# Performance work log

Measured on AMD Instinct MI355X. Metric: run time of the kernel, lower is better.

The kernel has to match this reference:

```python
import jax, jax.numpy as jnp
import numpy as np

N, H, T, HID = 2, 8, 1024, 64
EMBED_DIM = H * HID  # 512, out_proj dim
EPS = 1e-6


def setup_inputs() -> dict:
    key = jax.random.key(0)
    kq, kk, kv, kw, kb = jax.random.split(key, 5)
    q = jax.random.normal(kq, (N, H, T, HID), jnp.float32)
    k = jax.random.normal(kk, (N, H, T, HID), jnp.float32)
    v = jax.random.normal(kv, (N, H, T, HID), jnp.float32)
    W_out = jax.random.normal(kw, (EMBED_DIM, EMBED_DIM), jnp.float32) / np.float32(np.sqrt(EMBED_DIM))
    b_out = jax.random.normal(kb, (EMBED_DIM,), jnp.float32) * 0.02
    return {"q": q, "k": k, "v": v, "W_out": W_out, "b_out": b_out}


def reference(q, k, v, W_out, b_out):
    # cosFormer attention, causal=True, act_fun='relu', has_outproj=True
    n, h, t, hid = q.shape
    nh = n * h
    m = t  # max(src_len, tgt_len)

    # q/k: permute(2,0,1,3).view(T,N,H*HID) -> relu -> view(-1,N*H,HID).transpose(0,1)
    # is equivalent to a direct reshape (N,H,T,HID)->(N*H,T,HID) since relu is elementwise.
    qr = jax.nn.relu(q).reshape(nh, t, hid)
    kr = jax.nn.relu(k).reshape(nh, t, hid)
    # v: original does v.view(-1, N*H, HID).transpose(0,1) WITHOUT permuting first
    # (reinterprets the (N,H,T,HID) buffer as (T, N*H, HID)); reproduce faithfully.
    vr = jnp.swapaxes(v.reshape(t, nh, hid), 0, 1)  # (NH, T, HID)

    # cos/sin position reweighting: weight_index = pi/2 * arange(1..m), used as /m
    idx = (np.float32(np.pi / 2) * jnp.arange(1, t + 1, dtype=q.dtype)) / m  # (T,)
    s = jnp.sin(idx)[None, :, None]
    c = jnp.cos(idx)[None, :, None]
    q_ = jnp.concatenate([qr * s, qr * c], axis=-1)  # (NH, T, 2*HID)
    k_ = jnp.concatenate([kr * s, kr * c], axis=-1)  # (NH, T, 2*HID)

    # causal path: cumulative outer products k_ (x) v, then contract with q_
    kv = jnp.einsum('nld,nlm->nldm', k_, vr)          # (NH, T, 2*HID, HID)
    kv_cum = jnp.cumsum(kv, axis=1)
    qkv = jnp.einsum('nld,nldm->nlm', q_, kv_cum)     # (NH, T, HID)
    k_cum = jnp.cumsum(k_, axis=1)
    denom = jnp.maximum(jnp.einsum('nld,nld->nl', q_, k_cum), EPS)
    attn = qkv / denom[..., None]                     # (NH, T, HID)

    # (NH,T,HID) -> (T,N,H*HID), out_proj, back to (N,H,T,HID)
    attn = jnp.swapaxes(attn, 0, 1).reshape(t, n, h * hid)
    attn = attn @ W_out.T + b_out
    context = attn.reshape(t, n, h, hid).transpose(1, 2, 0, 3)  # (N,H,T,HID)
    probs = jnp.zeros((n, h, t, t), q.dtype)
    return context, probs
```

## Files before the change

### kernel.cpp

```cpp
#include <hip/hip_runtime.h>

#define TSEQ 1024
#define HIDV 64
#define NHEADS 16
#define LCH 64
#define NCH 16
#define EMBED 512
#define CTX_FLOATS (NHEADS * TSEQ * HIDV)
#define EPSV 1e-6f
#define PIH 1.5707963267948966f

typedef short bf16x8 __attribute__((ext_vector_type(8)));
typedef float f32x4 __attribute__((ext_vector_type(4)));

__device__ __forceinline__ float relu_f(float x) { return fmaxf(x, 0.0f); }
__device__ __forceinline__ ushort f2bf(float f) {
    uint u = __float_as_uint(f);
    u += 0x7FFF + ((u >> 16) & 1);
    return (ushort)(u >> 16);
}
__device__ __forceinline__ float bf2f(ushort h) { return __uint_as_float(((uint)h) << 16); }
__device__ __forceinline__ uint pk2(float a, float b) {
    return (uint)f2bf(a) | ((uint)f2bf(b) << 16);
}

__global__ __launch_bounds__(256) void kA_chunksum(
    const float* __restrict__ K, const float* __restrict__ V,
    const float* __restrict__ W,
    ushort* __restrict__ S16, float* __restrict__ ksumws,
    ushort* __restrict__ W16, float4* __restrict__ probs4)
{
    __shared__ ushort kwT[128 * 88];
    __shared__ ushort vT1[32 * 88];
    const int bid = blockIdx.x;
    const int tid = threadIdx.x;

    {
        float4 z = make_float4(0.f, 0.f, 0.f, 0.f);
        size_t base = (size_t)bid * 2560 + tid;
        #pragma unroll
        for (int s = 0; s < 10; ++s) probs4[base + s * 256] = z;
    }
    {
        int g = bid * 128 + (tid & 127);
        if (tid < 128) {
            float4 w4 = *(const float4*)(W + (size_t)g * 4);
            *(uint2*)(W16 + (size_t)g * 4) = make_uint2(pk2(w4.x, w4.y), pk2(w4.z, w4.w));
        }
    }

    const int pair = bid >> 1, mh = bid & 1, m0b = mh * 32;
    const int b = pair >> 4, c = pair & 15;
    const int l0 = c * LCH;

    #pragma unroll
    for (int s = 0; s < 4; ++s) {
        int e = tid + s * 256;
        int i = e >> 4, d = (e & 15) * 4;
        float4 k4 = *(const float4*)(K + (size_t)(b * TSEQ + l0 + i) * HIDV + d);
        float si, ci;
        __sincosf(PIH * (float)(l0 + i + 1) * (1.0f / 1024.0f), &si, &ci);
        float kv[4] = {relu_f(k4.x), relu_f(k4.y), relu_f(k4.z), relu_f(k4.w)};
        #pragma unroll
        for (int j = 0; j < 4; ++j) {
            kwT[(d + j) * 88 + i] = f2bf(si * kv[j]);
            kwT[(d + 64 + j) * 88 + i] = f2bf(ci * kv[j]);
        }
    }
    #pragma unroll
    for (int s = 0; s < 2; ++s) {
        int e = tid + s * 256;
        int i = e >> 3, mf = (e & 7) * 4;
        float4 v4 = *(const float4*)(V + ((size_t)(l0 + i) * NHEADS + b) * HIDV + m0b + mf);
        vT1[(mf + 0) * 88 + i] = f2bf(v4.x);
        vT1[(mf + 1) * 88 + i] = f2bf(v4.y);
        vT1[(mf + 2) * 88 + i] = f2bf(v4.z);
        vT1[(mf + 3) * 88 + i] = f2bf(v4.w);
    }
    __syncthreads();

    const int w = tid >> 6, lane = tid & 63;
    const int quad = lane >> 4, l15 = lane & 15;

    bf16x8 bfv[2][2];
    #pragma unroll
    for (int mt = 0; mt < 2; ++mt)
        #pragma unroll
        for (int kk = 0; kk < 2; ++kk)
            bfv[mt][kk] = *(const bf16x8*)(vT1 + (mt * 16 + l15) * 88 + kk * 32 + quad * 8);

    f32x4 acc[2][2];
    #pragma unroll
    for (int ii = 0; ii < 2; ++ii)
        #pragma unroll
        for (int mt = 0; mt < 2; ++mt) acc[ii][mt] = (f32x4){0.f, 0.f, 0.f, 0.f};
    #pragma unroll
    for (int ii = 0; ii < 2; ++ii) {
        int itv = w + ii * 4;
        #pragma unroll
        for (int kk = 0; kk < 2; ++kk) {
            bf16x8 af = *(const bf16x8*)(kwT + (itv * 16 + l15) * 88 + kk * 32 + quad * 8);
            #pragma unroll
            for (int mt = 0; mt < 2; ++mt)
                acc[ii][mt] = __builtin_amdgcn_mfma_f32_16x16x32_bf16(af, bfv[mt][kk], acc[ii][mt], 0, 0, 0);
        }
    }
    ushort* SpT = S16 + (size_t)pair * 8192;
    #pragma unroll
    for (int ii = 0; ii < 2; ++ii)
        #pragma unroll
        for (int mt = 0; mt < 2; ++mt) {
            int m = m0b + mt * 16 + l15;
            int ddb = (w + ii * 4) * 16 + quad * 4;
            uint2 pk = make_uint2(pk2(acc[ii][mt][0], acc[ii][mt][1]),
                                  pk2(acc[ii][mt][2], acc[ii][mt][3]));
            *(uint2*)(SpT + m * 128 + ddb) = pk;
        }
    if (mh == 0 && tid < 128) {
        float ssum = 0.f;
        #pragma unroll
        for (int ss = 0; ss < 8; ++ss) {
            uint4 u = *(const uint4*)(kwT + tid * 88 + ss * 8);
            ssum += bf2f((ushort)(u.x & 0xffff)) + bf2f((ushort)(u.x >> 16));
            ssum += bf2f((ushort)(u.y & 0xffff)) + bf2f((ushort)(u.y >> 16));
            ssum += bf2f((ushort)(u.z & 0xffff)) + bf2f((ushort)(u.z >> 16));
            ssum += bf2f((ushort)(u.w & 0xffff)) + bf2f((ushort)(u.w >> 16));
        }
        ksumws[(size_t)pair * 128 + tid] = ssum;
    }
}

#define SMEM_BYTES 58368
#define OFF_QW 0
#define OFF_KW 17408
#define OFF_PT 34816
#define OFF_VT 43520
#define OFF_AM 48128
#define OFF_PSUM 57344
#define OFF_DENA 57856
#define OFF_DENI 58112

__global__ __launch_bounds__(256) void kB_attn(
    const float* __restrict__ Q, const float* __restrict__ K,
    const float* __restrict__ V,
    const ushort* __restrict__ S16, const float* __restrict__ ksumws,
    ushort* __restrict__ attn216, float4* __restrict__ probs4)
{
    __shared__ __align__(16) char smem[SMEM_BYTES];
    ushort* qw = (ushort*)(smem + OFF_QW);
    ushort* kw = (ushort*)(smem + OFF_KW);
    ushort* Pt = (ushort*)(smem + OFF_PT);
    ushort* vT = (ushort*)(smem + OFF_VT);
    ushort* Am = (ushort*)(smem + OFF_AM);
    float* psum = (float*)(smem + OFF_PSUM);
    float* denA = (float*)(smem + OFF_DENA);
    float* denI = (float*)(smem + OFF_DENI);

    const int bid = blockIdx.x;
    const int tid = threadIdx.x;
    const int w = tid >> 6, lane = tid & 63;
    const int quad = lane >> 4, l15 = lane & 15;

    {
        float4 z = make_float4(0.f, 0.f, 0.f, 0.f);
        size_t base = 1310720 + (size_t)bid * 2560 + tid;
        #pragma unroll
        for (int s = 0; s < 10; ++s) probs4[base + s * 256] = z;
    }

    const int pair = bid >> 1, mh = bid & 1, m0b = mh * 32;
    const int b = pair >> 4, c = pair & 15;
    const int l0 = c * LCH;

    {
        const int ml = tid >> 3, dd0 = (tid & 7) * 16;
        const ushort* Sb = S16 + ((size_t)b * NCH) * 8192 + (m0b + ml) * 128 + dd0;
        float accp[16];
        #pragma unroll
        for (int u = 0; u < 16; ++u) accp[u] = 0.f;
        for (int cp = 0; cp < c; ++cp) {
            const ushort* Sp = Sb + (size_t)cp * 8192;
            uint4 u0 = *(const uint4*)(Sp);
            uint4 u1 = *(const uint4*)(Sp + 8);
            uint uu[8] = {u0.x, u0.y, u0.z, u0.w, u1.x, u1.y, u1.z, u1.w};
            #pragma unroll
            for (int p = 0; p < 8; ++p) {
                accp[p * 2 + 0] += bf2f((ushort)(uu[p] & 0xffff));
                accp[p * 2 + 1] += bf2f((ushort)(uu[p] >> 16));
            }
        }
        uint pkv[8];
        #pragma unroll
        for (int p = 0; p < 8; ++p) pkv[p] = pk2(accp[p * 2], accp[p * 2 + 1]);
        *(uint4*)(Pt + ml * 136 + dd0) = make_uint4(pkv[0], pkv[1], pkv[2], pkv[3]);
        *(uint4*)(Pt + ml * 136 + dd0 + 8) = make_uint4(pkv[4], pkv[5], pkv[6], pkv[7]);
    }
    if (tid < 128) {
        float s = 0.f;
        const float* Kb = ksumws + (size_t)b * NCH * 128 + tid;
        for (int cp = 0; cp < c; ++cp) s += Kb[cp * 128];
        psum[tid] = s;
    }

    #pragma unroll
    for (int s = 0; s < 4; ++s) {
        int e = tid + s * 256;
        int i = e >> 4, d = (e & 15) * 4;
        float si, ci;
        __sincosf(PIH * (float)(l0 + i + 1) * (1.0f / 1024.0f), &si, &ci);
        float4 q4 = *(const float4*)(Q + (size_t)(b * TSEQ + l0 + i) * HIDV + d);
        float qv[4] = {relu_f(q4.x), relu_f(q4.y), relu_f(q4.z), relu_f(q4.w)};
        *(uint2*)(qw + i * 136 + d) = make_uint2(pk2(si * qv[0], si * qv[1]), pk2(si * qv[2], si * qv[3]));
        *(uint2*)(qw + i * 136 + 64 + d) = make_uint2(pk2(ci * qv[0], ci * qv[1]), pk2(ci * qv[2], ci * qv[3]));
        float4 k4 = *(const float4*)(K + (size_t)(b * TSEQ + l0 + i) * HIDV + d);
        float kv[4] = {relu_f(k4.x), relu_f(k4.y), relu_f(k4.z), relu_f(k4.w)};
        *(uint2*)(kw + i * 136 + d) = make_uint2(pk2(si * kv[0], si * kv[1]), pk2(si * kv[2], si * kv[3]));
        *(uint2*)(kw + i * 136 + 64 + d) = make_uint2(pk2(ci * kv[0], ci * kv[1]), pk2(ci * kv[2], ci * kv[3]));
    }
    #pragma unroll
    for (int s = 0; s < 2; ++s) {
        int e = tid + s * 256;
        int j = e >> 3, mf = (e & 7) * 4;
        float4 v4 = *(const float4*)(V + ((size_t)(l0 + j) * NHEADS + b) * HIDV + m0b + mf);
        vT[(mf + 0) * 72 + j] = f2bf(v4.x);
        vT[(mf + 1) * 72 + j] = f2bf(v4.y);
        vT[(mf + 2) * 72 + j] = f2bf(v4.z);
        vT[(mf + 3) * 72 + j] = f2bf(v4.w);
    }
    __syncthreads();

    const int it = w;
    bf16x8 af[4];
    #pragma unroll
    for (int kk = 0; kk < 4; ++kk)
        af[kk] = *(const bf16x8*)(qw + (it * 16 + l15) * 136 + kk * 32 + quad * 8);

    f32x4 accA[4];
    #pragma unroll
    for (int jt = 0; jt < 4; ++jt) {
        accA[jt] = (f32x4){0.f, 0.f, 0.f, 0.f};
        #pragma unroll
        for (int kk = 0; kk < 4; ++kk) {
            bf16x8 bf = *(const bf16x8*)(kw + (jt * 16 + l15) * 136 + kk * 32 + quad * 8);
            accA[jt] = __builtin_amdgcn_mfma_f32_16x16x32_bf16(af[kk], bf, accA[jt], 0, 0, 0);
        }
    }
    {
        float rsum[4] = {0.f, 0.f, 0.f, 0.f};
        #pragma unroll
        for (int jt = 0; jt < 4; ++jt) {
            int j = jt * 16 + l15;
            #pragma unroll
            for (int r = 0; r < 4; ++r) {
                int i = it * 16 + quad * 4 + r;
                float val = (j <= i) ? accA[jt][r] : 0.f;
                Am[i * 72 + j] = f2bf(val);
                rsum[r] += val;
            }
        }
        #pragma unroll
        for (int off = 1; off < 16; off <<= 1) {
            rsum[0] += __shfl_xor(rsum[0], off);
            rsum[1] += __shfl_xor(rsum[1], off);
            rsum[2] += __shfl_xor(rsum[2], off);
            rsum[3] += __shfl_xor(rsum[3], off);
        }
        if (l15 == 0) {
            #pragma unroll
            for (int r = 0; r < 4; ++r) denA[it * 16 + quad * 4 + r] = rsum[r];
        }
    }
    if (tid < 64) {
        float s = 0.f;
        #pragma unroll
        for (int ss = 0; ss < 16; ++ss) {
            uint4 u = *(const uint4*)(qw + tid * 136 + ss * 8);
            s += bf2f((ushort)(u.x & 0xffff)) * psum[ss * 8 + 0] + bf2f((ushort)(u.x >> 16)) * psum[ss * 8 + 1];
            s += bf2f((ushort)(u.y & 0xffff)) * psum[ss * 8 + 2] + bf2f((ushort)(u.y >> 16)) * psum[ss * 8 + 3];
            s += bf2f((ushort)(u.z & 0xffff)) * psum[ss * 8 + 4] + bf2f((ushort)(u.z >> 16)) * psum[ss * 8 + 5];
            s += bf2f((ushort)(u.w & 0xffff)) * psum[ss * 8 + 6] + bf2f((ushort)(u.w >> 16)) * psum[ss * 8 + 7];
        }
        denI[tid] = s;
    }
    __syncthreads();

    f32x4 accO[2];
    #pragma unroll
    for (int mm = 0; mm < 2; ++mm) {
        accO[mm] = (f32x4){0.f, 0.f, 0.f, 0.f};
        #pragma unroll
        for (int kk = 0; kk < 4; ++kk) {
            bf16x8 bp = *(const bf16x8*)(Pt + (mm * 16 + l15) * 136 + kk * 32 + quad * 8);
            accO[mm] = __builtin_amdgcn_mfma_f32_16x16x32_bf16(af[kk], bp, accO[mm], 0, 0, 0);
        }
    }
    bf16x8 aA[2];
    #pragma unroll
    for (int kk = 0; kk < 2; ++kk)
        aA[kk] = *(const bf16x8*)(Am + (it * 16 + l15) * 72 + kk * 32 + quad * 8);
    #pragma unroll
    for (int mm = 0; mm < 2; ++mm)
        #pragma unroll
        for (int kk = 0; kk < 2; ++kk) {
            bf16x8 bv = *(const bf16x8*)(vT + (mm * 16 + l15) * 72 + kk * 32 + quad * 8);
            accO[mm] = __builtin_amdgcn_mfma_f32_16x16x32_bf16(aA[kk], bv, accO[mm], 0, 0, 0);
        }

    const int nb = b >> 3, hh = b & 7;
    #pragma unroll
    for (int r = 0; r < 4; ++r) {
        int i = it * 16 + quad * 4 + r;
        float inv = 1.0f / fmaxf(denA[i] + denI[i], EPSV);
        #pragma unroll
        for (int mm = 0; mm < 2; ++mm) {
            int m = m0b + mm * 16 + l15;
            attn216[(size_t)((l0 + i) * 2 + nb) * EMBED + hh * 64 + m] = f2bf(accO[mm][r] * inv);
        }
    }
}

__global__ __launch_bounds__(256) void kC_outproj(
    const ushort* __restrict__ A16, const ushort* __restrict__ W16,
    const float* __restrict__ bias, float* __restrict__ out,
    float4* __restrict__ probs4)
{
    __shared__ ushort Ab[32 * 72];
    __shared__ ushort Bb[64 * 72];
    const int bid = blockIdx.x;
    const int tid = threadIdx.x;
    {
        float4 z = make_float4(0.f, 0.f, 0.f, 0.f);
        size_t base = 2621440 + (size_t)bid * 3072 + tid;
        #pragma unroll
        for (int s = 0; s < 12; ++s) probs4[base + s * 256] = z;
    }
    const int rt = bid >> 3, et = bid & 7;
    const int r0 = rt * 32, e0 = et * 64;
    const int w = tid >> 6, lane = tid & 63;
    const int quad = lane >> 4, l15 = lane & 15;
    const int it4 = w >> 1, jt0 = (w & 1) * 2;
    f32x4 acc4[2];
    acc4[0] = (f32x4){0.f, 0.f, 0.f, 0.f};
    acc4[1] = (f32x4){0.f, 0.f, 0.f, 0.f};

    for (int f0 = 0; f0 < EMBED; f0 += 64) {
        __syncthreads();
        {
            int rr = tid >> 3, ff = (tid & 7) * 8;
            *(uint4*)(Ab + rr * 72 + ff) = *(const uint4*)(A16 + (size_t)(r0 + rr) * EMBED + f0 + ff);
        }
        #pragma unroll
        for (int s = 0; s < 2; ++s) {
            int e = tid + s * 256;
            int rr = e >> 3, ff = (e & 7) * 8;
            *(uint4*)(Bb + rr * 72 + ff) = *(const uint4*)(W16 + (size_t)(e0 + rr) * EMBED + f0 + ff);
        }
        __syncthreads();
        bf16x8 af2[2];
        #pragma unroll
        for (int kk = 0; kk < 2; ++kk)
            af2[kk] = *(const bf16x8*)(Ab + (it4 * 16 + l15) * 72 + kk * 32 + quad * 8);
        #pragma unroll
        for (int jj = 0; jj < 2; ++jj) {
            int jt = jt0 + jj;
            #pragma unroll
            for (int kk = 0; kk < 2; ++kk) {
                bf16x8 bf = *(const bf16x8*)(Bb + (jt * 16 + l15) * 72 + kk * 32 + quad * 8);
                acc4[jj] = __builtin_amdgcn_mfma_f32_16x16x32_bf16(af2[kk], bf, acc4[jj], 0, 0, 0);
            }
        }
    }
    #pragma unroll
    for (int jj = 0; jj < 2; ++jj) {
        int e = e0 + (jt0 + jj) * 16 + l15;
        float be = bias[e];
        int h = e >> 6, m = e & 63;
        #pragma unroll
        for (int r = 0; r < 4; ++r) {
            int rr = r0 + it4 * 16 + quad * 4 + r;
            int t = rr >> 1, n = rr & 1;
            out[((size_t)(n * 8 + h) * TSEQ + t) * HIDV + m] = acc4[jj][r] + be;
        }
    }
}

extern "C" void kernel_launch(void* const* d_in, const int* in_sizes, int n_in,
                              void* d_out, int out_size, void* d_ws, size_t ws_size,
                              hipStream_t stream) {
    const float* q = (const float*)d_in[0];
    const float* k = (const float*)d_in[1];
    const float* v = (const float*)d_in[2];
    const float* W = (const float*)d_in[3];
    const float* bias = (const float*)d_in[4];
    float* out = (float*)d_out;
    float* ws = (float*)d_ws;

    ushort* S16 = (ushort*)ws;
    float* ksum_ws = ws + 1048576;
    ushort* attn216 = (ushort*)(ws + 1081344);
    ushort* W16 = (ushort*)(ws + 1605632);
    float4* probs4 = (float4*)(out + CTX_FLOATS);

    kA_chunksum<<<dim3(512), dim3(256), 0, stream>>>(k, v, W, S16, ksum_ws, W16, probs4);
    kB_attn<<<dim3(512), dim3(256), 0, stream>>>(q, k, v, S16, ksum_ws, attn216, probs4);
    kC_outproj<<<dim3(512), dim3(256), 0, stream>>>(attn216, W16, bias, out, probs4);
}
```

Measured before the change: 115.0 us.

## Fuse three kernels into one cooperative kernel with grid syncs

Merges the chunk-sum, attention and out-projection kernels into a single cooperative launch, separated by grid.sync barriers. The K/Q/V tiles stay in LDS between the chunk-sum and attention phases instead of being reloaded. Attention output is staged through LDS so global stores are coalesced, and the zero-fill of probs and the final outputs use nontemporal stores. This removes two kernel launch gaps and the redundant K/V loads, but adds grid-wide barrier costs and requires all 512 blocks to be resident at once (launch_bounds 256,2).

Result: slower. 331.6 us (+188.3%).

```diff
diff --git a/kernel.cpp b/kernel.cpp
--- a/kernel.cpp
+++ b/kernel.cpp
@@ -1,4 +1,7 @@
 #include <hip/hip_runtime.h>
+#include <hip/hip_cooperative_groups.h>
+
+namespace cg = cooperative_groups;
 
 #define TSEQ 1024
 #define HIDV 64
@@ -24,22 +27,46 @@
     return (uint)f2bf(a) | ((uint)f2bf(b) << 16);
 }
 
-__global__ __launch_bounds__(256) void kA_chunksum(
-    const float* __restrict__ K, const float* __restrict__ V,
-    const float* __restrict__ W,
+#define LDS_BYTES 62976
+#define OFF_KW   0
+#define OFF_VT   17408
+#define OFF_R3   23040
+#define OFF_R4   45568
+#define OFF_PT   (OFF_R3 + 0)
+#define OFF_AM   (OFF_R3 + 8704)
+#define OFF_PSUM (OFF_R3 + 17920)
+#define OFF_DENA (OFF_R3 + 18432)
+#define OFF_DENI (OFF_R3 + 18688)
+
+__global__ __launch_bounds__(256, 2) void kFused(
+    const float* __restrict__ Q, const float* __restrict__ K,
+    const float* __restrict__ V, const float* __restrict__ W,
+    const float* __restrict__ bias,
     ushort* __restrict__ S16, float* __restrict__ ksumws,
-    ushort* __restrict__ W16, float4* __restrict__ probs4)
+    ushort* __restrict__ attn216, ushort* __restrict__ W16,
+    float* __restrict__ out, float4* __restrict__ probs4)
 {
-    __shared__ ushort kwT[128 * 88];
-    __shared__ ushort vT1[32 * 88];
+    __shared__ __align__(16) char smem[LDS_BYTES];
+    ushort* kw = (ushort*)(smem + OFF_KW);
+    ushort* vT = (ushort*)(smem + OFF_VT);
+    ushort* qw = (ushort*)(smem + OFF_R4);
+
     const int bid = blockIdx.x;
     const int tid = threadIdx.x;
-
-    {
-        float4 z = make_float4(0.f, 0.f, 0.f, 0.f);
+    const int w = tid >> 6, lane = tid & 63;
+    const int quad = lane >> 4, l15 = lane & 15;
+    const int pair = bid >> 1, mh = bid & 1, m0b = mh * 32;
+    const int b = pair >> 4, c = pair & 15;
+    const int l0 = c * LCH;
+
+    cg::grid_group grid = cg::this_grid();
+
+    {
+        f32x4 z = {0.f, 0.f, 0.f, 0.f};
         size_t base = (size_t)bid * 2560 + tid;
         #pragma unroll
-        for (int s = 0; s < 10; ++s) probs4[base + s * 256] = z;
+        for (int s = 0; s < 10; ++s)
+            __builtin_nontemporal_store(z, (f32x4*)&probs4[base + s * 256]);
     }
     {
         int g = bid * 128 + (tid & 127);
@@ -48,338 +75,289 @@
             *(uint2*)(W16 + (size_t)g * 4) = make_uint2(pk2(w4.x, w4.y), pk2(w4.z, w4.w));
         }
     }
-
-    const int pair = bid >> 1, mh = bid & 1, m0b = mh * 32;
-    const int b = pair >> 4, c = pair & 15;
-    const int l0 = c * LCH;
-
-    #pragma unroll
-    for (int s = 0; s < 4; ++s) {
-        int e = tid + s * 256;
-        int i = e >> 4, d = (e & 15) * 4;
-        float4 k4 = *(const float4*)(K + (size_t)(b * TSEQ + l0 + i) * HIDV + d);
-        float si, ci;
-        __sincosf(PIH * (float)(l0 + i + 1) * (1.0f / 1024.0f), &si, &ci);
-        float kv[4] = {relu_f(k4.x), relu_f(k4.y), relu_f(k4.z), relu_f(k4.w)};
-        #pragma unroll
-        for (int j = 0; j < 4; ++j) {
-            kwT[(d + j) * 88 + i] = f2bf(si * kv[j]);
-            kwT[(d + 64 + j) * 88 + i] = f2bf(ci * kv[j]);
-        }
-    }
-    #pragma unroll
-    for (int s = 0; s < 2; ++s) {
-        int e = tid + s * 256;
-        int i = e >> 3, mf = (e & 7) * 4;
-        float4 v4 = *(const float4*)(V + ((size_t)(l0 + i) * NHEADS + b) * HIDV + m0b + mf);
-        vT1[(mf + 0) * 88 + i] = f2bf(v4.x);
-        vT1[(mf + 1) * 88 + i] = f2bf(v4.y);
-        vT1[(mf + 2) * 88 + i] = f2bf(v4.z);
-        vT1[(mf + 3) * 88 + i] = f2bf(v4.w);
-    }
-    __syncthreads();
-
-    const int w = tid >> 6, lane = tid & 63;
-    const int quad = lane >> 4, l15 = lane & 15;
-
-    bf16x8 bfv[2][2];
-    #pragma unroll
-    for (int mt = 0; mt < 2; ++mt)
-        #pragma unroll
-        for (int kk = 0; kk < 2; ++kk)
-            bfv[mt][kk] = *(const bf16x8*)(vT1 + (mt * 16 + l15) * 88 + kk * 32 + quad * 8);
-
-    f32x4 acc[2][2];
-    #pragma unroll
-    for (int ii = 0; ii < 2; ++ii)
-        #pragma unroll
-        for (int mt = 0; mt < 2; ++mt) acc[ii][mt] = (f32x4){0.f, 0.f, 0.f, 0.f};
-    #pragma unroll
-    for (int ii = 0; ii < 2; ++ii) {
-        int itv = w + ii * 4;
-        #pragma unroll
-        for (int kk = 0; kk < 2; ++kk) {
-            bf16x8 af = *(const bf16x8*)(kwT + (itv * 16 + l15) * 88 + kk * 32 + quad * 8);
-            #pragma unroll
-            for (int mt = 0; mt < 2; ++mt)
-                acc[ii][mt] = __builtin_amdgcn_mfma_f32_16x16x32_bf16(af, bfv[mt][kk], acc[ii][mt], 0, 0, 0);
-        }
-    }
-    ushort* SpT = S16 + (size_t)pair * 8192;
-    #pragma unroll
-    for (int ii = 0; ii < 2; ++ii)
-        #pragma unroll
-        for (int mt = 0; mt < 2; ++mt) {
-            int m = m0b + mt * 16 + l15;
-            int ddb = (w + ii * 4) * 16 + quad * 4;
-            uint2 pk = make_uint2(pk2(acc[ii][mt][0], acc[ii][mt][1]),
-                                  pk2(acc[ii][mt][2], acc[ii][mt][3]));
-            *(uint2*)(SpT + m * 128 + ddb) = pk;
-        }
-    if (mh == 0 && tid < 128) {
-        float ssum = 0.f;
-        #pragma unroll
-        for (int ss = 0; ss < 8; ++ss) {
-            uint4 u = *(const uint4*)(kwT + tid * 88 + ss * 8);
-            ssum += bf2f((ushort)(u.x & 0xffff)) + bf2f((ushort)(u.x >> 16));
-            ssum += bf2f((ushort)(u.y & 0xffff)) + bf2f((ushort)(u.y >> 16));
-            ssum += bf2f((ushort)(u.z & 0xffff)) + bf2f((ushort)(u.z >> 16));
-            ssum += bf2f((ushort)(u.w & 0xffff)) + bf2f((ushort)(u.w >> 16));
-        }
-        ksumws[(size_t)pair * 128 + tid] = ssum;
-    }
-}
-
-#define SMEM_BYTES 58368
-#define OFF_QW 0
-#define OFF_KW 17408
-#define OFF_PT 34816
-#define OFF_VT 43520
-#define OFF_AM 48128
-#define OFF_PSUM 57344
-#define OFF_DENA 57856
-#define OFF_DENI 58112
-
-__global__ __launch_bounds__(256) void kB_attn(
-    const float* __restrict__ Q, const float* __restrict__ K,
-    const float* __restrict__ V,
-    const ushort* __restrict__ S16, const float* __restrict__ ksumws,
-    ushort* __restrict__ attn216, float4* __restrict__ probs4)
-{
-    __shared__ __align__(16) char smem[SMEM_BYTES];
-    ushort* qw = (ushort*)(smem + OFF_QW);
-    ushort* kw = (ushort*)(smem + OFF_KW);
-    ushort* Pt = (ushort*)(smem + OFF_PT);
-    ushort* vT = (ushort*)(smem + OFF_VT);
-    ushort* Am = (ushort*)(smem + OFF_AM);
-    float* psum = (float*)(smem + OFF_PSUM);
-    float* denA = (float*)(smem + OFF_DENA);
-    float* denI = (float*)(smem + OFF_DENI);
-
-    const int bid = blockIdx.x;
-    const int tid = threadIdx.x;
-    const int w = tid >> 6, lane = tid & 63;
-    const int quad = lane >> 4, l15 = lane & 15;
-
-    {
-        float4 z = make_float4(0.f, 0.f, 0.f, 0.f);
-        size_t base = 1310720 + (size_t)bid * 2560 + tid;
-        #pragma unroll
-        for (int s = 0; s < 10; ++s) probs4[base + s * 256] = z;
-    }
-
-    const int pair = bid >> 1, mh = bid & 1, m0b = mh * 32;
-    const int b = pair >> 4, c = pair & 15;
-    const int l0 = c * LCH;
-
-    {
-        const int ml = tid >> 3, dd0 = (tid & 7) * 16;
-        const ushort* Sb = S16 + ((size_t)b * NCH) * 8192 + (m0b + ml) * 128 + dd0;
-        float accp[16];
-        #pragma unroll
-        for (int u = 0; u < 16; ++u) accp[u] = 0.f;
-        for (int cp = 0; cp < c; ++cp) {
-            const ushort* Sp = Sb + (size_t)cp * 8192;
-            uint4 u0 = *(const uint4*)(Sp);
-            uint4 u1 = *(const uint4*)(Sp + 8);
-            uint uu[8] = {u0.x, u0.y, u0.z, u0.w, u1.x, u1.y, u1.z, u1.w};
-            #pragma unroll
-            for (int p = 0; p < 8; ++p) {
-                accp[p * 2 + 0] += bf2f((ushort)(uu[p] & 0xffff));
-                accp[p * 2 + 1] += bf2f((ushort)(uu[p] >> 16));
-            }
-        }
-        uint pkv[8];
-        #pragma unroll
-        for (int p = 0; p < 8; ++p) pkv[p] = pk2(accp[p * 2], accp[p * 2 + 1]);
-        *(uint4*)(Pt + ml * 136 + dd0) = make_uint4(pkv[0], pkv[1], pkv[2], pkv[3]);
-        *(uint4*)(Pt + ml * 136 + dd0 + 8) = make_uint4(pkv[4], pkv[5], pkv[6], pkv[7]);
-    }
-    if (tid < 128) {
-        float s = 0.f;
-        const float* Kb = ksumws + (size_t)b * NCH * 128 + tid;
-        for (int cp = 0; cp < c; ++cp) s += Kb[cp * 128];
-        psum[tid] = s;
-    }
-
-    #pragma unroll
-    for (int s = 0; s < 4; ++s) {
-        int e = tid + s * 256;
-        int i = e >> 4, d = (e & 15) * 4;
-        float si, ci;
-        __sincosf(PIH * (float)(l0 + i + 1) * (1.0f / 1024.0f), &si, &ci);
-        float4 q4 = *(const float4*)(Q + (size_t)(b * TSEQ + l0 + i) * HIDV + d);
-        float qv[4] = {relu_f(q4.x), relu_f(q4.y), relu_f(q4.z), relu_f(q4.w)};
-        *(uint2*)(qw + i * 136 + d) = make_uint2(pk2(si * qv[0], si * qv[1]), pk2(si * qv[2], si * qv[3]));
-        *(uint2*)(qw + i * 136 + 64 + d) = make_uint2(pk2(ci * qv[0], ci * qv[1]), pk2(ci * qv[2], ci * qv[3]));
-        float4 k4 = *(const float4*)(K + (size_t)(b * TSEQ + l0 + i) * HIDV + d);
-        float kv[4] = {relu_f(k4.x), relu_f(k4.y), relu_f(k4.z), relu_f(k4.w)};
-        *(uint2*)(kw + i * 136 + d) = make_uint2(pk2(si * kv[0], si * kv[1]), pk2(si * kv[2], si * kv[3]));
-        *(uint2*)(kw + i * 136 + 64 + d) = make_uint2(pk2(ci * kv[0], ci * kv[1]), pk2(ci * kv[2], ci * kv[3]));
-    }
-    #pragma unroll
-    for (int s = 0; s < 2; ++s) {
-        int e = tid + s * 256;
-        int j = e >> 3, mf = (e & 7) * 4;
-        float4 v4 = *(const float4*)(V + ((size_t)(l0 + j) * NHEADS + b) * HIDV + m0b + mf);
-        vT[(mf + 0) * 72 + j] = f2bf(v4.x);
-        vT[(mf + 1) * 72 + j] = f2bf(v4.y);
-        vT[(mf + 2) * 72 + j] = f2bf(v4.z);
-        vT[(mf + 3) * 72 + j] = f2bf(v4.w);
-    }
-    __syncthreads();
-
-    const int it = w;
-    bf16x8 af[4];
-    #pragma unroll
-    for (int kk = 0; kk < 4; ++kk)
-        af[kk] = *(const bf16x8*)(qw + (it * 16 + l15) * 136 + kk * 32 + quad * 8);
-
-    f32x4 accA[4];
-    #pragma unroll
-    for (int jt = 0; jt < 4; ++jt) {
-        accA[jt] = (f32x4){0.f, 0.f, 0.f, 0.f};
-        #pragma unroll
-        for (int kk = 0; kk < 4; ++kk) {
-            bf16x8 bf = *(const bf16x8*)(kw + (jt * 16 + l15) * 136 + kk * 32 + quad * 8);
-            accA[jt] = __builtin_amdgcn_mfma_f32_16x16x32_bf16(af[kk], bf, accA[jt], 0, 0, 0);
-        }
-    }
-    {
-        float rsum[4] = {0.f, 0.f, 0.f, 0.f};
-        #pragma unroll
-        for (int jt = 0; jt < 4; ++jt) {
-            int j = jt * 16 + l15;
-            #pragma unroll
-            for (int r = 0; r < 4; ++r) {
-                int i = it * 16 + quad * 4 + r;
-                float val = (j <= i) ? accA[jt][r] : 0.f;
-                Am[i * 72 + j] = f2bf(val);
-                rsum[r] += val;
-            }
-        }
-        #pragma unroll
-        for (int off = 1; off < 16; off <<= 1) {
-            rsum[0] += __shfl_xor(rsum[0], off);
-            rsum[1] += __shfl_xor(rsum[1], off);
-            rsum[2] += __shfl_xor(rsum[2], off);
-            rsum[3] += __shfl_xor(rsum[3], off);
-        }
-        if (l15 == 0) {
-            #pragma unroll
-            for (int r = 0; r < 4; ++r) denA[it * 16 + quad * 4 + r] = rsum[r];
-        }
-    }
-    if (tid < 64) {
-        float s = 0.f;
-        #pragma unroll
-        for (int ss = 0; ss < 16; ++ss) {
-            uint4 u = *(const uint4*)(qw + tid * 136 + ss * 8);
-            s += bf2f((ushort)(u.x & 0xffff)) * psum[ss * 8 + 0] + bf2f((ushort)(u.x >> 16)) * psum[ss * 8 + 1];
-            s += bf2f((ushort)(u.y & 0xffff)) * psum[ss * 8 + 2] + bf2f((ushort)(u.y >> 16)) * psum[ss * 8 + 3];
-            s += bf2f((ushort)(u.z & 0xffff)) * psum[ss * 8 + 4] + bf2f((ushort)(u.z >> 16)) * psum[ss * 8 + 5];
-            s += bf2f((ushort)(u.w & 0xffff)) * psum[ss * 8 + 6] + bf2f((ushort)(u.w >> 16)) * psum[ss * 8 + 7];
-        }
-        denI[tid] = s;
-    }
-    __syncthreads();
-
-    f32x4 accO[2];
-    #pragma unroll
-    for (int mm = 0; mm < 2; ++mm) {
-        accO[mm] = (f32x4){0.f, 0.f, 0.f, 0.f};
-        #pragma unroll
-        for (int kk = 0; kk < 4; ++kk) {
-            bf16x8 bp = *(const bf16x8*)(Pt + (mm * 16 + l15) * 136 + kk * 32 + quad * 8);
-            accO[mm] = __builtin_amdgcn_mfma_f32_16x16x32_bf16(af[kk], bp, accO[mm], 0, 0, 0);
-        }
-    }
-    bf16x8 aA[2];
-    #pragma unroll
-    for (int kk = 0; kk < 2; ++kk)
-        aA[kk] = *(const bf16x8*)(Am + (it * 16 + l15) * 72 + kk * 32 + quad * 8);
-    #pragma unroll
-    for (int mm = 0; mm < 2; ++mm)
-        #pragma unroll
-        for (int kk = 0; kk < 2; ++kk) {
-            bf16x8 bv = *(const bf16x8*)(vT + (mm * 16 + l15) * 72 + kk * 32 + quad * 8);
-            accO[mm] = __builtin_amdgcn_mfma_f32_16x16x32_bf16(aA[kk], bv, accO[mm], 0, 0, 0);
-        }
-
-    const int nb = b >> 3, hh = b & 7;
-    #pragma unroll
-    for (int r = 0; r < 4; ++r) {
-        int i = it * 16 + quad * 4 + r;
-        float inv = 1.0f / fmaxf(denA[i] + denI[i], EPSV);
-        #pragma unroll
-        for (int mm = 0; mm < 2; ++mm) {
-            int m = m0b + mm * 16 + l15;
-            attn216[(size_t)((l0 + i) * 2 + nb) * EMBED + hh * 64 + m] = f2bf(accO[mm][r] * inv);
-        }
-    }
-}
-
-__global__ __launch_bounds__(256) void kC_outproj(
-    const ushort* __restrict__ A16, const ushort* __restrict__ W16,
-    const float* __restrict__ bias, float* __restrict__ out,
-    float4* __restrict__ probs4)
-{
-    __shared__ ushort Ab[32 * 72];
-    __shared__ ushort Bb[64 * 72];
-    const int bid = blockIdx.x;
-    const int tid = threadIdx.x;
-    {
-        float4 z = make_float4(0.f, 0.f, 0.f, 0.f);
-        size_t base = 2621440 + (size_t)bid * 3072 + tid;
-        #pragma unroll
-        for (int s = 0; s < 12; ++s) probs4[base + s * 256] = z;
-    }
-    const int rt = bid >> 3, et = bid & 7;
-    const int r0 = rt * 32, e0 = et * 64;
-    const int w = tid >> 6, lane = tid & 63;
-    const int quad = lane >> 4, l15 = lane & 15;
-    const int it4 = w >> 1, jt0 = (w & 1) * 2;
-    f32x4 acc4[2];
-    acc4[0] = (f32x4){0.f, 0.f, 0.f, 0.f};
-    acc4[1] = (f32x4){0.f, 0.f, 0.f, 0.f};
-
-    for (int f0 = 0; f0 < EMBED; f0 += 64) {
-        __syncthreads();
-        {
-            int rr = tid >> 3, ff = (tid & 7) * 8;
-            *(uint4*)(Ab + rr * 72 + ff) = *(const uint4*)(A16 + (size_t)(r0 + rr) * EMBED + f0 + ff);
+    {
+        ushort* kwT = (ushort*)(smem + OFF_R3);
+        #pragma unroll
+        for (int s = 0; s < 4; ++s) {
+            int e = tid + s * 256;
+            int i = e >> 4, d = (e & 15) * 4;
+            float si, ci;
+            __sincosf(PIH * (float)(l0 + i + 1) * (1.0f / 1024.0f), &si, &ci);
+            float4 k4 = *(const float4*)(K + (size_t)(b * TSEQ + l0 + i) * HIDV + d);
+            float kv[4] = {relu_f(k4.x), relu_f(k4.y), relu_f(k4.z), relu_f(k4.w)};
+            #pragma unroll
+            for (int j = 0; j < 4; ++j) {
+                kwT[(d + j) * 88 + i] = f2bf(si * kv[j]);
+                kwT[(d + 64 + j) * 88 + i] = f2bf(ci * kv[j]);
+            }
+            *(uint2*)(kw + i * 136 + d) = make_uint2(pk2(si * kv[0], si * kv[1]), pk2(si * kv[2], si * kv[3]));
+            *(uint2*)(kw + i * 136 + 64 + d) = make_uint2(pk2(ci * kv[0], ci * kv[1]), pk2(ci * kv[2], ci * kv[3]));
+            float4 q4 = *(const float4*)(Q + (size_t)(b * TSEQ + l0 + i) * HIDV + d);
+            float qv[4] = {relu_f(q4.x), relu_f(q4.y), relu_f(q4.z), relu_f(q4.w)};
+            *(uint2*)(qw + i * 136 + d) = make_uint2(pk2(si * qv[0], si * qv[1]), pk2(si * qv[2], si * qv[3]));
+            *(uint2*)(qw + i * 136 + 64 + d) = make_uint2(pk2(ci * qv[0], ci * qv[1]), pk2(ci * qv[2], ci * qv[3]));
         }
         #pragma unroll
         for (int s = 0; s < 2; ++s) {
             int e = tid + s * 256;
-            int rr = e >> 3, ff = (e & 7) * 8;
-            *(uint4*)(Bb + rr * 72 + ff) = *(const uint4*)(W16 + (size_t)(e0 + rr) * EMBED + f0 + ff);
+            int i = e >> 3, mf = (e & 7) * 4;
+            float4 v4 = *(const float4*)(V + ((size_t)(l0 + i) * NHEADS + b) * HIDV + m0b + mf);
+            vT[(mf + 0) * 88 + i] = f2bf(v4.x);
+            vT[(mf + 1) * 88 + i] = f2bf(v4.y);
+            vT[(mf + 2) * 88 + i] = f2bf(v4.z);
+            vT[(mf + 3) * 88 + i] = f2bf(v4.w);
         }
         __syncthreads();
-        bf16x8 af2[2];
+
+        bf16x8 bfv[2][2];
+        #pragma unroll
+        for (int mt = 0; mt < 2; ++mt)
+            #pragma unroll
+            for (int kk = 0; kk < 2; ++kk)
+                bfv[mt][kk] = *(const bf16x8*)(vT + (mt * 16 + l15) * 88 + kk * 32 + quad * 8);
+
+        f32x4 acc[2][2];
+        #pragma unroll
+        for (int ii = 0; ii < 2; ++ii)
+            #pragma unroll
+            for (int mt = 0; mt < 2; ++mt) acc[ii][mt] = (f32x4){0.f, 0.f, 0.f, 0.f};
+        #pragma unroll
+        for (int ii = 0; ii < 2; ++ii) {
+            int itv = w + ii * 4;
+            #pragma unroll
+            for (int kk = 0; kk < 2; ++kk) {
+                bf16x8 af = *(const bf16x8*)(kwT + (itv * 16 + l15) * 88 + kk * 32 + quad * 8);
+                #pragma unroll
+                for (int mt = 0; mt < 2; ++mt)
+                    acc[ii][mt] = __builtin_amdgcn_mfma_f32_16x16x32_bf16(af, bfv[mt][kk], acc[ii][mt], 0, 0, 0);
+            }
+        }
+        ushort* SpT = S16 + (size_t)pair * 8192;
+        #pragma unroll
+        for (int ii = 0; ii < 2; ++ii)
+            #pragma unroll
+            for (int mt = 0; mt < 2; ++mt) {
+                int m = m0b + mt * 16 + l15;
+                int ddb = (w + ii * 4) * 16 + quad * 4;
+                uint2 pk = make_uint2(pk2(acc[ii][mt][0], acc[ii][mt][1]),
+                                      pk2(acc[ii][mt][2], acc[ii][mt][3]));
+                *(uint2*)(SpT + m * 128 + ddb) = pk;
+            }
+        if (mh == 0 && tid < 128) {
+            float ssum = 0.f;
+            #pragma unroll
+            for (int ss = 0; ss < 8; ++ss) {
+                uint4 u = *(const uint4*)(kwT + tid * 88 + ss * 8);
+                ssum += bf2f((ushort)(u.x & 0xffff)) + bf2f((ushort)(u.x >> 16));
+                ssum += bf2f((ushort)(u.y & 0xffff)) + bf2f((ushort)(u.y >> 16));
+                ssum += bf2f((ushort)(u.z & 0xffff)) + bf2f((ushort)(u.z >> 16));
+                ssum += bf2f((ushort)(u.w & 0xffff)) + bf2f((ushort)(u.w >> 16));
+            }
+            ksumws[(size_t)pair * 128 + tid] = ssum;
+        }
+    }
+    __threadfence();
+    grid.sync();
+
+    {
+        ushort* Pt = (ushort*)(smem + OFF_PT);
+        ushort* Am = (ushort*)(smem + OFF_AM);
+        float* psum = (float*)(smem + OFF_PSUM);
+        float* denA = (float*)(smem + OFF_DENA);
+        float* denI = (float*)(smem + OFF_DENI);
+
+        {
+            f32x4 z = {0.f, 0.f, 0.f, 0.f};
+            size_t base = 1310720 + (size_t)bid * 2560 + tid;
+            #pragma unroll
+            for (int s = 0; s < 10; ++s)
+                __builtin_nontemporal_store(z, (f32x4*)&probs4[base + s * 256]);
+        }
+
+        {
+            const int ml = tid >> 3, dd0 = (tid & 7) * 16;
+            const ushort* Sb = S16 + ((size_t)b * NCH) * 8192 + (m0b + ml) * 128 + dd0;
+            float accp[16];
+            #pragma unroll
+            for (int u = 0; u < 16; ++u) accp[u] = 0.f;
+            for (int cp = 0; cp < c; ++cp) {
+                const ushort* Sp = Sb + (size_t)cp * 8192;
+                uint4 u0 = *(const uint4*)(Sp);
+                uint4 u1 = *(const uint4*)(Sp + 8);
+                uint uu[8] = {u0.x, u0.y, u0.z, u0.w, u1.x, u1.y, u1.z, u1.w};
+                #pragma unroll
+                for (int p = 0; p < 8; ++p) {
+                    accp[p * 2 + 0] += bf2f((ushort)(uu[p] & 0xffff));
+                    accp[p * 2 + 1] += bf2f((ushort)(uu[p] >> 16));
+                }
+            }
+            uint pkv[8];
+            #pragma unroll
+            for (int p = 0; p < 8; ++p) pkv[p] = pk2(accp[p * 2], accp[p * 2 + 1]);
+            *(uint4*)(Pt + ml * 136 + dd0) = make_uint4(pkv[0], pkv[1], pkv[2], pkv[3]);
+            *(uint4*)(Pt + ml * 136 + dd0 + 8) = make_uint4(pkv[4], pkv[5], pkv[6], pkv[7]);
+        }
+        if (tid < 128) {
+            float s = 0.f;
+            const float* Kb = ksumws + (size_t)b * NCH * 128 + tid;
+            for (int cp = 0; cp < c; ++cp) s += Kb[cp * 128];
+            psum[tid] = s;
+        }
+
+        bf16x8 af[4];
+        #pragma unroll
+        for (int kk = 0; kk < 4; ++kk)
+            af[kk] = *(const bf16x8*)(qw + (w * 16 + l15) * 136 + kk * 32 + quad * 8);
+
+        __syncthreads();
+
+        f32x4 accA[4];
+        #pragma unroll
+        for (int jt = 0; jt < 4; ++jt) {
+            accA[jt] = (f32x4){0.f, 0.f, 0.f, 0.f};
+            #pragma unroll
+            for (int kk = 0; kk < 4; ++kk) {
+                bf16x8 bf = *(const bf16x8*)(kw + (jt * 16 + l15) * 136 + kk * 32 + quad * 8);
+                accA[jt] = __builtin_amdgcn_mfma_f32_16x16x32_bf16(af[kk], bf, accA[jt], 0, 0, 0);
+            }
+        }
+        {
+            float rsum[4] = {0.f, 0.f, 0.f, 0.f};
+            #pragma unroll
+            for (int jt = 0; jt < 4; ++jt) {
+                int j = jt * 16 + l15;
+                #pragma unroll
+                for (int r = 0; r < 4; ++r) {
+                    int i = w * 16 + quad * 4 + r;
+                    float val = (j <= i) ? accA[jt][r] : 0.f;
+                    Am[i * 72 + j] = f2bf(val);
+                    rsum[r] += val;
+                }
+            }
+            #pragma unroll
+            for (int off = 1; off < 16; off <<= 1) {
+                rsum[0] += __shfl_xor(rsum[0], off);
+                rsum[1] += __shfl_xor(rsum[1], off);
+                rsum[2] += __shfl_xor(rsum[2], off);
+                rsum[3] += __shfl_xor(rsum[3], off);
+            }
+            if (l15 == 0) {
+                #pragma unroll
+                for (int r = 0; r < 4; ++r) denA[w * 16 + quad * 4 + r] = rsum[r];
+            }
+        }
+        if (tid < 64) {
+            float s = 0.f;
+            #pragma unroll
+            for (int ss = 0; ss < 16; ++ss) {
+                uint4 u = *(const uint4*)(qw + tid * 136 + ss * 8);
+                s += bf2f((ushort)(u.x & 0xffff)) * psum[ss * 8 + 0] + bf2f((ushort)(u.x >> 16)) * psum[ss * 8 + 1];
+                s += bf2f((ushort)(u.y & 0xffff)) * psum[ss * 8 + 2] + bf2f((ushort)(u.y >> 16)) * psum[ss * 8 + 3];
+                s += bf2f((ushort)(u.z & 0xffff)) * psum[ss * 8 + 4] + bf2f((ushort)(u.z >> 16)) * psum[ss * 8 + 5];
+                s += bf2f((ushort)(u.w & 0xffff)) * psum[ss * 8 + 6] + bf2f((ushort)(u.w >> 16)) * psum[ss * 8 + 7];
+            }
+            denI[tid] = s;
+        }
+        __syncthreads();
+
+        f32x4 accO[2];
+        #pragma unroll
+        for (int mm = 0; mm < 2; ++mm) {
+            accO[mm] = (f32x4){0.f, 0.f, 0.f, 0.f};
+            #pragma unroll
+            for (int kk = 0; kk < 4; ++kk) {
+                bf16x8 bp = *(const bf16x8*)(Pt + (mm * 16 + l15) * 136 + kk * 32 + quad * 8);
+                accO[mm] = __builtin_amdgcn_mfma_f32_16x16x32_bf16(af[kk], bp, accO[mm], 0, 0, 0);
+            }
+        }
+        bf16x8 aA[2];
         #pragma unroll
         for (int kk = 0; kk < 2; ++kk)
-            af2[kk] = *(const bf16x8*)(Ab + (it4 * 16 + l15) * 72 + kk * 32 + quad * 8);
+            aA[kk] = *(const bf16x8*)(Am + (w * 16 + l15) * 72 + kk * 32 + quad * 8);
+        #pragma unroll
+        for (int mm = 0; mm < 2; ++mm)
+            #pragma unroll
+            for (int kk = 0; kk < 2; ++kk) {
+                bf16x8 bv = *(const bf16x8*)(vT + (mm * 16 + l15) * 88 + kk * 32 + quad * 8);
+                accO[mm] = __builtin_amdgcn_mfma_f32_16x16x32_bf16(aA[kk], bv, accO[mm], 0, 0, 0);
+            }
+
+        ushort* Orep = (ushort*)(smem + OFF_R4);
+        const int nb = b >> 3, hh = b & 7;
+        #pragma unroll
+        for (int r = 0; r < 4; ++r) {
+            int i = w * 16 + quad * 4 + r;
+            float inv = 1.0f / fmaxf(denA[i] + denI[i], EPSV);
+            #pragma unroll
+            for (int mm = 0; mm < 2; ++mm)
+                Orep[i * 40 + mm * 16 + l15] = f2bf(accO[mm][r] * inv);
+        }
+        __syncthreads();
+        {
+            int rr = tid >> 2, f = (tid & 3) * 8;
+            uint4 vv = *(const uint4*)(Orep + rr * 40 + f);
+            *(uint4*)(attn216 + (size_t)((l0 + rr) * 2 + nb) * EMBED + hh * 64 + m0b + f) = vv;
+        }
+    }
+    __threadfence();
+    grid.sync();
+
+    {
+        ushort* Ab = (ushort*)(smem + OFF_R4);
+        ushort* Bb = (ushort*)(smem + OFF_R4 + 4608);
+        {
+            f32x4 z = {0.f, 0.f, 0.f, 0.f};
+            size_t base = 2621440 + (size_t)bid * 3072 + tid;
+            #pragma unroll
+            for (int s = 0; s < 12; ++s)
+                __builtin_nontemporal_store(z, (f32x4*)&probs4[base + s * 256]);
+        }
+        const int rt = bid >> 3, et = bid & 7;
+        const int r0 = rt * 32, e0 = et * 64;
+        const int it4 = w >> 1, jt0 = (w & 1) * 2;
+        f32x4 acc4[2];
+        acc4[0] = (f32x4){0.f, 0.f, 0.f, 0.f};
+        acc4[1] = (f32x4){0.f, 0.f, 0.f, 0.f};
+
+        for (int f0 = 0; f0 < EMBED; f0 += 64) {
+            __syncthreads();
+            {
+                int rr = tid >> 3, ff = (tid & 7) * 8;
+                *(uint4*)(Ab + rr * 72 + ff) = *(const uint4*)(attn216 + (size_t)(r0 + rr) * EMBED + f0 + ff);
+            }
+            #pragma unroll
+            for (int s = 0; s < 2; ++s) {
+                int e = tid + s * 256;
+                int rr = e >> 3, ff = (e & 7) * 8;
+                *(uint4*)(Bb + rr * 72 + ff) = *(const uint4*)(W16 + (size_t)(e0 + rr) * EMBED + f0 + ff);
+            }
+            __syncthreads();
+            bf16x8 af2[2];
+            #pragma unroll
+            for (int kk = 0; kk < 2; ++kk)
+                af2[kk] = *(const bf16x8*)(Ab + (it4 * 16 + l15) * 72 + kk * 32 + quad * 8);
+            #pragma unroll
+            for (int jj = 0; jj < 2; ++jj) {
+                int jt = jt0 + jj;
+                #pragma unroll
+                for (int kk = 0; kk < 2; ++kk) {
+                    bf16x8 bf = *(const bf16x8*)(Bb + (jt * 16 + l15) * 72 + kk * 32 + quad * 8);
+                    acc4[jj] = __builtin_amdgcn_mfma_f32_16x16x32_bf16(af2[kk], bf, acc4[jj], 0, 0, 0);
+                }
+            }
+        }
         #pragma unroll
         for (int jj = 0; jj < 2; ++jj) {
-            int jt = jt0 + jj;
-            #pragma unroll
-            for (int kk = 0; kk < 2; ++kk) {
-                bf16x8 bf = *(const bf16x8*)(Bb + (jt * 16 + l15) * 72 + kk * 32 + quad * 8);
-                acc4[jj] = __builtin_amdgcn_mfma_f32_16x16x32_bf16(af2[kk], bf, acc4[jj], 0, 0, 0);
-            }
-        }
-    }
-    #pragma unroll
-    for (int jj = 0; jj < 2; ++jj) {
-        int e = e0 + (jt0 + jj) * 16 + l15;
-        float be = bias[e];
-        int h = e >> 6, m = e & 63;
-        #pragma unroll
-        for (int r = 0; r < 4; ++r) {
-            int rr = r0 + it4 * 16 + quad * 4 + r;
-            int t = rr >> 1, n = rr & 1;
-            out[((size_t)(n * 8 + h) * TSEQ + t) * HIDV + m] = acc4[jj][r] + be;
+            int e = e0 + (jt0 + jj) * 16 + l15;
+            float be = bias[e];
+            int h = e >> 6, m = e & 63;
+            #pragma unroll
+            for (int r = 0; r < 4; ++r) {
+                int rr = r0 + it4 * 16 + quad * 4 + r;
+                int t = rr >> 1, n = rr & 1;
+                __builtin_nontemporal_store(acc4[jj][r] + be,
+                    &out[((size_t)(n * 8 + h) * TSEQ + t) * HIDV + m]);
+            }
         }
     }
 }
@@ -401,7 +379,8 @@
     ushort* W16 = (ushort*)(ws + 1605632);
     float4* probs4 = (float4*)(out + CTX_FLOATS);
 
-    kA_chunksum<<<dim3(512), dim3(256), 0, stream>>>(k, v, W, S16, ksum_ws, W16, probs4);
-    kB_attn<<<dim3(512), dim3(256), 0, stream>>>(q, k, v, S16, ksum_ws, attn216, probs4);
-    kC_outproj<<<dim3(512), dim3(256), 0, stream>>>(attn216, W16, bias, out, probs4);
+    void* args[] = {(void*)&q, (void*)&k, (void*)&v, (void*)&W, (void*)&bias,
+                    (void*)&S16, (void*)&ksum_ws, (void*)&attn216, (void*)&W16,
+                    (void*)&out, (void*)&probs4};
+    hipLaunchCooperativeKernel((void*)kFused, dim3(512), dim3(256), args, 0, stream);
 }
```
